# Performance work log

Measured on AMD Instinct MI355X. Metric: run time of the kernel, lower is better.

## Reference

```python
import jax, jax.numpy as jnp
import numpy as np

B = 8192   # batch
S = 115    # state dim (fixed by slice layout)
E = 3072   # retrieval embed dim
C = 128    # compressed context dim
A = 23     # action dim
NE = 4096  # number of hyperedge keys
K = 10     # top-k retrieval
TAU = 1.0  # gumbel temperature
EPS = 1e-5 # layernorm eps


def _ln(x, g, b):
    m = x.mean(-1, keepdims=True)
    v = x.var(-1, keepdims=True)
    return (x - m) * jax.lax.rsqrt(v + EPS) * g + b


def _actor(ctx, extra, w1, b1, g1, be1, w2, b2, g2, be2, w3, b3):
    x = jnp.concatenate([ctx, extra], -1)
    x = jax.nn.relu(_ln(x @ w1 + b1, g1, be1))
    x = jax.nn.relu(_ln(x @ w2 + b2, g2, be2))
    return x @ w3 + b3


def setup_inputs() -> dict:
    key = jax.random.key(0)
    ks = iter(jax.random.split(key, 80))

    def W(shape):
        return jax.random.normal(next(ks), shape, jnp.float32) * (1.0 / float(np.sqrt(shape[0])))

    inp = {}
    inp["state"] = jax.random.normal(next(ks), (B, S), jnp.float32)
    u = jax.random.uniform(next(ks), (B, 4), jnp.float32, 1e-6, 1.0 - 1e-6)
    inp["gumbel_noise"] = -jnp.log(-jnp.log(u))  # standard Gumbel samples
    inp["keys"] = jax.random.normal(next(ks), (NE, E), jnp.float32)
    # state encoder 115 -> 512 -> 512 -> 3072 + LN
    inp["se_w1"] = W((S, 512)); inp["se_b1"] = jnp.zeros(512)
    inp["se_w2"] = W((512, 512)); inp["se_b2"] = jnp.zeros(512)
    inp["se_w3"] = W((512, E)); inp["se_b3"] = jnp.zeros(E)
    inp["se_g"] = jnp.ones(E); inp["se_beta"] = jnp.zeros(E)
    # context compressor 3072 -> 512 -> 128 + LN
    inp["cc_w1"] = W((E, 512)); inp["cc_b1"] = jnp.zeros(512)
    inp["cc_w2"] = W((512, C)); inp["cc_b2"] = jnp.zeros(C)
    inp["cc_g"] = jnp.ones(C); inp["cc_beta"] = jnp.zeros(C)
    # 4 actor experts, differing only in extra-slice width
    for p, e in [("a_pre", 50), ("a_scene", 20), ("a_effect", 10), ("a_rule", 15)]:
        inp[p + "_w1"] = W((C + e, C)); inp[p + "_b1"] = jnp.zeros(C)
        inp[p + "_g1"] = jnp.ones(C); inp[p + "_be1"] = jnp.zeros(C)
        inp[p + "_w2"] = W((C, C)); inp[p + "_b2"] = jnp.zeros(C)
        inp[p + "_g2"] = jnp.ones(C); inp[p + "_be2"] = jnp.zeros(C)
        inp[p + "_w3"] = W((C, A)) * 0.01; inp[p + "_b3"] = jnp.zeros(A)  # orthogonal gain=0.01 approx
    # gumbel router 115 -> 64 -> 64 -> 4
    inp["r_w1"] = W((S, 64)); inp["r_b1"] = jnp.zeros(64)
    inp["r_w2"] = W((64, 64)); inp["r_b2"] = jnp.zeros(64)
    inp["r_w3"] = W((64, 4)); inp["r_b3"] = jnp.zeros(4)
    # critic 115 -> 256 -> 256 -> 1
    inp["c_w1"] = W((S, 256)); inp["c_b1"] = jnp.zeros(256)
    inp["c_w2"] = W((256, 256)); inp["c_b2"] = jnp.zeros(256)
    inp["c_w3"] = W((256, 1)); inp["c_b3"] = jnp.zeros(1)
    return inp


def reference(state, gumbel_noise, keys, se_w1, se_b1, se_w2, se_b2, se_w3, se_b3, se_g, se_beta, cc_w1, cc_b1, cc_w2, cc_b2, cc_g, cc_beta, a_pre_w1, a_pre_b1, a_pre_g1, a_pre_be1, a_pre_w2, a_pre_b2, a_pre_g2, a_pre_be2, a_pre_w3, a_pre_b3, a_scene_w1, a_scene_b1, a_scene_g1, a_scene_be1, a_scene_w2, a_scene_b2, a_scene_g2, a_scene_be2, a_scene_w3, a_scene_b3, a_effect_w1, a_effect_b1, a_effect_g1, a_effect_be1, a_effect_w2, a_effect_b2, a_effect_g2, a_effect_be2, a_effect_w3, a_effect_b3, a_rule_w1, a_rule_b1, a_rule_g1, a_rule_be1, a_rule_w2, a_rule_b2, a_rule_g2, a_rule_be2, a_rule_w3, a_rule_b3, r_w1, r_b1, r_w2, r_b2, r_w3, r_b3, c_w1, c_b1, c_w2, c_b2, c_w3, c_b3):
    # 1) state -> query (StateEncoder)
    q = jax.nn.relu(state @ se_w1 + se_b1)
    q = jax.nn.relu(q @ se_w2 + se_b2)
    q = _ln(q @ se_w3 + se_b3, se_g, se_beta)  # (B, E)
    # 2) top-k hard retrieval from hypergraph memory (cosine sim)
    qn = q * jax.lax.rsqrt(jnp.sum(q * q, -1, keepdims=True) + 1e-12)
    kn = keys * jax.lax.rsqrt(jnp.sum(keys * keys, -1, keepdims=True) + 1e-12)
    scores = qn @ kn.T                          # (B, NE)
    _, idx = jax.lax.top_k(scores, K)           # (B, K)
    context = jnp.take(keys, idx, axis=0).mean(1)  # (B, E) mean-pool top-k raw embeddings
    # 3) compress to shared knowledge
    h = jax.nn.relu(context @ cc_w1 + cc_b1)
    shared = _ln(h @ cc_w2 + cc_b2, cc_g, cc_beta)  # (B, C)
    # 4) state slices + 4 actor experts
    belief = state[:, :50]
    location = state[:, 20:40]
    hp = state[:, 40:50]
    inv = state[:, 45:60]
    lp = _actor(shared, belief, a_pre_w1, a_pre_b1, a_pre_g1, a_pre_be1, a_pre_w2, a_pre_b2, a_pre_g2, a_pre_be2, a_pre_w3, a_pre_b3)
    ls = _actor(shared, location, a_scene_w1, a_scene_b1, a_scene_g1, a_scene_be1, a_scene_w2, a_scene_b2, a_scene_g2, a_scene_be2, a_scene_w3, a_scene_b3)
    le = _actor(shared, hp, a_effect_w1, a_effect_b1, a_effect_g1, a_effect_be1, a_effect_w2, a_effect_b2, a_effect_g2, a_effect_be2, a_effect_w3, a_effect_b3)
    lr = _actor(shared, inv, a_rule_w1, a_rule_b1, a_rule_g1, a_rule_be1, a_rule_w2, a_rule_b2, a_rule_g2, a_rule_be2, a_rule_w3, a_rule_b3)
    # 5) gumbel-softmax hard router (straight-through)
    rh = jax.nn.relu(state @ r_w1 + r_b1)
    rh = jax.nn.relu(rh @ r_w2 + r_b2)
    rl = jnp.clip(rh @ r_w3 + r_b3, -20.0, 20.0)
    y_soft = jax.nn.softmax((rl + gumbel_noise) / TAU, -1)
    y_hard = jax.nn.one_hot(jnp.argmax(y_soft, -1), 4, dtype=y_soft.dtype)
    alpha = y_soft + jax.lax.stop_gradient(y_hard - y_soft)  # (B, 4)
    # 6) combine expert logits
    all_l = jnp.stack([lp, ls, le, lr], 1)      # (B, 4, A)
    logits = jnp.einsum('bk,bka->ba', alpha, all_l)
    # critic value
    v = jax.nn.relu(state @ c_w1 + c_b1)
    v = jax.nn.relu(v @ c_w2 + c_b2)
    value = v @ c_w3 + c_b3                      # (B, 1)
    return (logits, alpha, value)
```

## Files before the change

### kernel.cpp

```cpp
#include <hip/hip_runtime.h>

constexpr int Bz = 8192;
constexpr int Sz = 115;
constexpr int Ez = 3072;
constexpr int NEz = 4096;

typedef __attribute__((ext_vector_type(8))) short short8;
typedef __attribute__((ext_vector_type(4))) float floatx4;
typedef unsigned short ushort_t;
typedef unsigned int uint_t;

__device__ __forceinline__ ushort_t f2bf(float f) {
  uint_t u = __float_as_uint(f);
  uint_t r = (u + 0x7FFFu + ((u >> 16) & 1u)) >> 16;
  return (ushort_t)r;
}
__device__ __forceinline__ float bf2f(ushort_t b) {
  uint_t u = ((uint_t)b) << 16;
  return __uint_as_float(u);
}
__device__ __forceinline__ ushort_t f2key(float v) {
  _Float16 h = (_Float16)v;
  ushort_t b = __builtin_bit_cast(ushort_t, h);
  return b ^ ((b & 0x8000u) ? 0xFFFFu : 0x8000u);
}
__device__ __forceinline__ uint_t umax_(uint_t a, uint_t b) { return a > b ? a : b; }

__device__ __forceinline__ void gload16(const ushort_t* g, ushort_t* l) {
  __builtin_amdgcn_global_load_lds(
      (__attribute__((address_space(1))) const void*)g,
      (__attribute__((address_space(3))) void*)l, 16, 0, 0);
}

template<bool RELU, bool BIAS>
__global__ __launch_bounds__(256)
void gemm128(const float* __restrict__ A, const float* __restrict__ Bm,
             const float* __restrict__ bias, float* __restrict__ C,
             int N, int Kd)
{
  __shared__ float As[16][132];
  __shared__ float Bs[16][132];
  const int t  = threadIdx.x;
  const int tx = t & 15, ty = t >> 4;
  const int row0 = blockIdx.y * 128;
  const int col0 = blockIdx.x * 128;
  const int ar = t >> 2, ac = (t & 3) * 4;
  const int bk = t >> 5, bc = (t & 31) * 4;
  const bool a4 = (Kd & 3) == 0;

  float acc[8][8];
#pragma unroll
  for (int i = 0; i < 8; ++i)
#pragma unroll
    for (int j = 0; j < 8; ++j) acc[i][j] = 0.f;

  for (int k0 = 0; k0 < Kd; k0 += 16) {
    const bool fullA = (k0 + 16 <= Kd) && a4;
    {
      const float* ap = A + (size_t)(row0 + ar) * Kd + k0 + ac;
      if (fullA) {
        float4 v0 = *(const float4*)ap;
        float4 v1 = *(const float4*)(ap + (size_t)64 * Kd);
        As[ac + 0][ar] = v0.x; As[ac + 1][ar] = v0.y;
        As[ac + 2][ar] = v0.z; As[ac + 3][ar] = v0.w;
        As[ac + 0][ar + 64] = v1.x; As[ac + 1][ar + 64] = v1.y;
        As[ac + 2][ar + 64] = v1.z; As[ac + 3][ar + 64] = v1.w;
      } else {
#pragma unroll
        for (int e = 0; e < 4; ++e) {
          const int k = k0 + ac + e;
          float v0 = 0.f, v1 = 0.f;
          if (k < Kd) { v0 = ap[e]; v1 = ap[e + (size_t)64 * Kd]; }
          As[ac + e][ar] = v0; As[ac + e][ar + 64] = v1;
        }
      }
    }
    {
      const float* bp = Bm + (size_t)(k0 + bk) * N + col0 + bc;
      if (k0 + 16 <= Kd) {
        *(float4*)&Bs[bk][bc]     = *(const float4*)bp;
        *(float4*)&Bs[bk + 8][bc] = *(const float4*)(bp + (size_t)8 * N);
      } else {
        float4 z; z.x = z.y = z.z = z.w = 0.f;
        *(float4*)&Bs[bk][bc]     = (k0 + bk     < Kd) ? *(const float4*)bp : z;
        *(float4*)&Bs[bk + 8][bc] = (k0 + bk + 8 < Kd) ? *(const float4*)(bp + (size_t)8 * N) : z;
      }
    }
    __syncthreads();
#pragma unroll
    for (int kk = 0; kk < 16; ++kk) {
      float a[8], b[8];
      *(float4*)&a[0] = *(const float4*)&As[kk][ty * 4];
      *(float4*)&a[4] = *(const float4*)&As[kk][64 + ty * 4];
      *(float4*)&b[0] = *(const float4*)&Bs[kk][tx * 4];
      *(float4*)&b[4] = *(const float4*)&Bs[kk][64 + tx * 4];
#pragma unroll
      for (int i = 0; i < 8; ++i)
#pragma unroll
        for (int j = 0; j < 8; ++j)
          acc[i][j] = fmaf(a[i], b[j], acc[i][j]);
    }
    __syncthreads();
  }

  float bv[8];
#pragma unroll
  for (int j = 0; j < 8; ++j) bv[j] = 0.f;
  if (BIAS) {
    *(float4*)&bv[0] = *(const float4*)&bias[col0 + tx * 4];
    *(float4*)&bv[4] = *(const float4*)&bias[col0 + 64 + tx * 4];
  }
#pragma unroll
  for (int i = 0; i < 8; ++i) {
    const int r = row0 + ((i < 4) ? (ty * 4 + i) : (64 + ty * 4 + i - 4));
    float o[8];
#pragma unroll
    for (int j = 0; j < 8; ++j) {
      o[j] = acc[i][j] + bv[j];
      if (RELU) o[j] = fmaxf(o[j], 0.f);
    }
    *(float4*)&C[(size_t)r * N + col0 + tx * 4]      = *(float4*)&o[0];
    *(float4*)&C[(size_t)r * N + col0 + 64 + tx * 4] = *(float4*)&o[4];
  }
}

struct GPart {
  const float* A; const float* Bm; const float* bias;
  float* C; ushort_t* Ch; ushort_t* Cl;
  int N; int Kd; int nbx;
};

__global__ __launch_bounds__(256)
void gemm128_dual(GPart g0, GPart g1)
{
  __shared__ float As[16][132];
  __shared__ float Bs[16][132];
  const int t  = threadIdx.x;
  const int tx = t & 15, ty = t >> 4;
  const bool p0 = (int)blockIdx.x < g0.nbx;
  GPart g = p0 ? g0 : g1;
  const int bx = p0 ? blockIdx.x : (blockIdx.x - g0.nbx);
  const int row0 = blockIdx.y * 128;
  const int col0 = bx * 128;
  const int Kd = g.Kd, N = g.N;
  const int ar = t >> 2, ac = (t & 3) * 4;
  const int bk = t >> 5, bc = (t & 31) * 4;
  const bool a4 = (Kd & 3) == 0;

  float acc[8][8];
#pragma unroll
  for (int i = 0; i < 8; ++i)
#pragma unroll
    for (int j = 0; j < 8; ++j) acc[i][j] = 0.f;

  for (int k0 = 0; k0 < Kd; k0 += 16) {
    const bool fullA = (k0 + 16 <= Kd) && a4;
    {
      const float* ap = g.A + (size_t)(row0 + ar) * Kd + k0 + ac;
      if (fullA) {
        float4 v0 = *(const float4*)ap;
        float4 v1 = *(const float4*)(ap + (size_t)64 * Kd);
        As[ac + 0][ar] = v0.x; As[ac + 1][ar] = v0.y;
        As[ac + 2][ar] = v0.z; As[ac + 3][ar] = v0.w;
        As[ac + 0][ar + 64] = v1.x; As[ac + 1][ar + 64] = v1.y;
        As[ac + 2][ar + 64] = v1.z; As[ac + 3][ar + 64] = v1.w;
      } else {
#pragma unroll
        for (int e = 0; e < 4; ++e) {
          const int k = k0 + ac + e;
          float v0 = 0.f, v1 = 0.f;
          if (k < Kd) { v0 = ap[e]; v1 = ap[e + (size_t)64 * Kd]; }
          As[ac + e][ar] = v0; As[ac + e][ar + 64] = v1;
        }
      }
    }
    {
      const float* bp = g.Bm + (size_t)(k0 + bk) * N + col0 + bc;
      if (k0 + 16 <= Kd) {
        *(float4*)&Bs[bk][bc]     = *(const float4*)bp;
        *(float4*)&Bs[bk + 8][bc] = *(const float4*)(bp + (size_t)8 * N);
      } else {
        float4 z; z.x = z.y = z.z = z.w = 0.f;
        *(float4*)&Bs[bk][bc]     = (k0 + bk     < Kd) ? *(const float4*)bp : z;
        *(float4*)&Bs[bk + 8][bc] = (k0 + bk + 8 < Kd) ? *(const float4*)(bp + (size_t)8 * N) : z;
      }
    }
    __syncthreads();
#pragma unroll
    for (int kk = 0; kk < 16; ++kk) {
      float a[8], b[8];
      *(float4*)&a[0] = *(const float4*)&As[kk][ty * 4];
      *(float4*)&a[4] = *(const float4*)&As[kk][64 + ty * 4];
      *(float4*)&b[0] = *(const float4*)&Bs[kk][tx * 4];
      *(float4*)&b[4] = *(const float4*)&Bs[kk][64 + tx * 4];
#pragma unroll
      for (int i = 0; i < 8; ++i)
#pragma unroll
        for (int j = 0; j < 8; ++j)
          acc[i][j] = fmaf(a[i], b[j], acc[i][j]);
    }
    __syncthreads();
  }

  float bv[8];
  *(float4*)&bv[0] = *(const float4*)&g.bias[col0 + tx * 4];
  *(float4*)&bv[4] = *(const float4*)&g.bias[col0 + 64 + tx * 4];
#pragma unroll
  for (int i = 0; i < 8; ++i) {
    const int r = row0 + ((i < 4) ? (ty * 4 + i) : (64 + ty * 4 + i - 4));
    float o[8];
#pragma unroll
    for (int j = 0; j < 8; ++j) o[j] = fmaxf(acc[i][j] + bv[j], 0.f);
    const size_t i0 = (size_t)r * N + col0 + tx * 4;
    const size_t i1 = i0 + 64;
    if (g.C) {
      *(float4*)&g.C[i0] = *(float4*)&o[0];
      *(float4*)&g.C[i1] = *(float4*)&o[4];
    }
    if (g.Ch) {
      ushort4 h0, l0, h1, l1;
      h0.x = f2bf(o[0]); l0.x = f2bf(o[0] - bf2f(h0.x));
      h0.y = f2bf(o[1]); l0.y = f2bf(o[1] - bf2f(h0.y));
      h0.z = f2bf(o[2]); l0.z = f2bf(o[2] - bf2f(h0.z));
      h0.w = f2bf(o[3]); l0.w = f2bf(o[3] - bf2f(h0.w));
      h1.x = f2bf(o[4]); l1.x = f2bf(o[4] - bf2f(h1.x));
      h1.y = f2bf(o[5]); l1.y = f2bf(o[5] - bf2f(h1.y));
      h1.z = f2bf(o[6]); l1.z = f2bf(o[6] - bf2f(h1.z));
      h1.w = f2bf(o[7]); l1.w = f2bf(o[7] - bf2f(h1.w));
      *(ushort4*)&g.Ch[i0] = h0; *(ushort4*)&g.Cl[i0] = l0;
      *(ushort4*)&g.Ch[i1] = h1; *(ushort4*)&g.Cl[i1] = l1;
    }
  }
}

__global__ __launch_bounds__(512, 2)
void screen256(const ushort_t* __restrict__ A, const ushort_t* __restrict__ B,
               ushort_t* __restrict__ Cout, int N, int Kd)
{
  __shared__ ushort_t AL[2 * 256 * 64];
  __shared__ ushort_t BL[2 * 256 * 64];
  const int t = threadIdx.x;
  const int lane = t & 63;
  const int wid = t >> 6;
  const int wr = wid >> 2;
  const int wc = wid & 3;
  const int mr = lane & 15, qd = lane >> 4;
  const int row0 = (int)blockIdx.y << 8;
  const int col0 = (int)blockIdx.x << 8;
  const int NT = Kd >> 6;

  const int l8 = lane >> 3;
  const int c8 = (lane & 7) ^ l8;
  const ushort_t* pA = A + (size_t)(row0 + wr * 128 + wc * 16 + l8) * Kd + c8 * 8;
  const ushort_t* pB = B + (size_t)(col0 + (wid >> 1) * 64 + (wid & 1) * 16 + l8) * Kd + c8 * 8;
  ushort_t* aWp = &AL[wr * 8192 + wc * 1024];
  ushort_t* bWp = &BL[(wid >> 1) * 4096 + (wid & 1) * 1024];

  const int swz = (mr & 7) << 4;
  const int aRow = (wr * 128 + mr) * 64;
  const int bRow = (wc * 64 + mr) * 64;
  const int cu0 = ((qd * 16) ^ swz) >> 1;
  const int cu1 = ((64 + qd * 16) ^ swz) >> 1;

  floatx4 acc[8][4];
#pragma unroll
  for (int i = 0; i < 8; ++i)
#pragma unroll
    for (int j = 0; j < 4; ++j) acc[i][j] = (floatx4){0.f, 0.f, 0.f, 0.f};

  short8 A0r[4][2], A1r[4][2], B0r[2][2], B1r[2][2];

#define STA(db, h, tile) do {                                            \
    const int kt_ = ((tile) < NT ? (tile) : 0) << 6;                     \
    gload16(pA + (size_t)((h) * 64) * Kd + kt_,                          \
            aWp + (db) * 16384 + (h) * 4096);                            \
    gload16(pA + (size_t)((h) * 64 + 8) * Kd + kt_,                      \
            aWp + (db) * 16384 + (h) * 4096 + 512);                      \
  } while (0)
#define STB(db, g, tile) do {                                            \
    const int kt_ = ((tile) < NT ? (tile) : 0) << 6;                     \
    gload16(pB + (size_t)((g) * 32) * Kd + kt_,                          \
            bWp + (db) * 16384 + (g) * 2048);                            \
    gload16(pB + (size_t)((g) * 32 + 8) * Kd + kt_,                      \
            bWp + (db) * 16384 + (g) * 2048 + 512);                      \
  } while (0)
#define LDAm(dst, db, half)                                              \
  _Pragma("unroll")                                                      \
  for (int i_ = 0; i_ < 4; ++i_) {                                       \
    const int b_ = (db) * 16384 + aRow + ((half) * 4 + i_) * 1024;       \
    dst[i_][0] = *(const short8*)&AL[b_ + cu0];                          \
    dst[i_][1] = *(const short8*)&AL[b_ + cu1];                          \
  }
#define LDBm(dst, db, jh)                                                \
  _Pragma("unroll")                                                      \
  for (int j_ = 0; j_ < 2; ++j_) {                                       \
    const int b_ = (db) * 16384 + bRow + ((jh) * 2 + j_) * 1024;         \
    dst[j_][0] = *(const short8*)&BL[b_ + cu0];                          \
    dst[j_][1] = *(const short8*)&BL[b_ + cu1];                          \
  }
#define MMq(ih, jh, As_, Bs_)                                            \
  _Pragma("unroll")                                                      \
  for (int s_ = 0; s_ < 2; ++s_)                                         \
    _Pragma("unroll")                                                    \
    for (int i_ = 0; i_ < 4; ++i_)                                       \
      _Pragma("unroll")                                                  \
      for (int j_ = 0; j_ < 2; ++j_)                                     \
        acc[(ih)*4+i_][(jh)*2+j_] = __builtin_amdgcn_mfma_f32_16x16x32_bf16( \
            As_[i_][s_], Bs_[j_][s_], acc[(ih)*4+i_][(jh)*2+j_], 0, 0, 0);
#define BARM() do { __builtin_amdgcn_s_barrier();                        \
                    asm volatile("" ::: "memory"); } while (0)
#define WLG()  do { asm volatile("s_waitcnt lgkmcnt(0)" ::: "memory");   \
                    __builtin_amdgcn_sched_barrier(0); } while (0)
#define WVM(n) asm volatile("s_waitcnt vmcnt(" #n ")" ::: "memory")
#define PRIO1() __builtin_amdgcn_s_setprio(1)
#define PRIO0() __builtin_amdgcn_s_setprio(0)
#define PHASE(ih, jh, As_, Bs_, READS)                                   \
  do {                                                                   \
    __builtin_amdgcn_s_barrier(); WLG();                                 \
    PRIO1(); MMq(ih, jh, As_, Bs_); PRIO0();                             \
    READS;                                                               \
    BARM();                                                              \
  } while (0)

  STA(0, 0, 0); STB(0, 0, 0); STB(0, 1, 0); STA(0, 1, 0);
  STA(1, 0, 1); STB(1, 0, 1); STB(1, 1, 1); STA(1, 1, 1);
  WVM(8);
  BARM();
  LDAm(A0r, 0, 0); LDBm(B0r, 0, 0);

  for (int it = 0; it < NT / 2; ++it) {
    const int tp = it * 2;
    PHASE(0, 0, A0r, B0r, LDBm(B1r, 0, 1));
    STA(0, 0, tp + 2); STB(0, 0, tp + 2);
    PHASE(0, 1, A0r, B1r, LDAm(A1r, 0, 1));
    STB(0, 1, tp + 2);
    WVM(6);
    PHASE(1, 1, A1r, B1r, LDAm(A0r, 1, 0));
    STA(0, 1, tp + 2);
    PHASE(1, 0, A1r, B0r, LDBm(B1r, 1, 0));
    PHASE(0, 0, A0r, B1r, LDBm(B0r, 1, 1));
    STA(1, 0, tp + 3); STB(1, 0, tp + 3);
    PHASE(0, 1, A0r, B0r, LDAm(A1r, 1, 1));
    STB(1, 1, tp + 3);
    WVM(6);
    PHASE(1, 1, A1r, B0r, LDAm(A0r, 0, 0));
    STA(1, 1, tp + 3);
    PHASE(1, 0, A1r, B1r, LDBm(B0r, 0, 0));
  }

  asm volatile("s_waitcnt vmcnt(0) lgkmcnt(0)" ::: "memory");
  __syncthreads();

#undef STA
#undef STB
#undef LDAm
#undef LDBm
#undef MMq
#undef PHASE
#undef BARM
#undef WLG
#undef WVM
#undef PRIO1
#undef PRIO0

#pragma unroll
  for (int i = 0; i < 8; ++i) {
#pragma unroll
    for (int j = 0; j < 4; ++j) {
      const int col = col0 + wc * 64 + j * 16 + mr;
#pragma unroll
      for (int r = 0; r < 4; ++r) {
        const int row = row0 + wr * 128 + i * 16 + qd * 4 + r;
        Cout[(size_t)row * N + col] = f2key(acc[i][j][r]);
      }
    }
  }
}

template<int EPI>
__global__ __launch_bounds__(256)
void mfma3_bt(const ushort_t* __restrict__ Ah, const ushort_t* __restrict__ Alo,
              const ushort_t* __restrict__ Bh, const ushort_t* __restrict__ Blo,
              const float* __restrict__ bias, float* __restrict__ Cout,
              ushort_t* __restrict__ Ch, ushort_t* __restrict__ Cl,
              int N, int Kd)
{
  __shared__ ushort_t AhL[128 * 32];
  __shared__ ushort_t AlL[128 * 32];
  __shared__ ushort_t BhL[128 * 32];
  __shared__ ushort_t BlL[128 * 32];
  const int t = threadIdx.x;
  const int wid = t >> 6, lane = t & 63;
  const int wr = wid >> 1, wc = wid & 1;
  const int row0 = blockIdx.y * 128;
  const int col0 = blockIdx.x * 128;
  const int srow = lane >> 2;
  const int scol = (lane & 3) * 8;

  const size_t aoff0 = (size_t)(row0 + wid * 16 + srow) * Kd + scol;
  const size_t aoff1 = (size_t)(row0 + (wid + 4) * 16 + srow) * Kd + scol;
  const size_t boff0 = (size_t)(col0 + wid * 16 + srow) * Kd + scol;
  const size_t boff1 = (size_t)(col0 + (wid + 4) * 16 + srow) * Kd + scol;
  const int l0 = (wid * 16) * 32;
  const int l1 = ((wid + 4) * 16) * 32;

  const int mr = lane & 15, qd = lane >> 4;

  floatx4 acc[4][4];
#pragma unroll
  for (int i = 0; i < 4; ++i)
#pragma unroll
    for (int j = 0; j < 4; ++j) acc[i][j] = (floatx4){0.f, 0.f, 0.f, 0.f};

  for (int kb = 0; kb < Kd; kb += 32) {
    gload16(Ah + aoff0 + kb, &AhL[l0]);
    gload16(Ah + aoff1 + kb, &AhL[l1]);
    gload16(Alo + aoff0 + kb, &AlL[l0]);
    gload16(Alo + aoff1 + kb, &AlL[l1]);
    gload16(Bh + boff0 + kb, &BhL[l0]);
    gload16(Bh + boff1 + kb, &BhL[l1]);
    gload16(Blo + boff0 + kb, &BlL[l0]);
    gload16(Blo + boff1 + kb, &BlL[l1]);
    __syncthreads();
    short8 ahF[4], alF[4], bhF[4], blF[4];
#pragma unroll
    for (int i = 0; i < 4; ++i) {
      const int o = (wr * 64 + i * 16 + mr) * 32 + qd * 8;
      ahF[i] = *(const short8*)&AhL[o];
      alF[i] = *(const short8*)&AlL[o];
    }
#pragma unroll
    for (int j = 0; j < 4; ++j) {
      const int o = (wc * 64 + j * 16 + mr) * 32 + qd * 8;
      bhF[j] = *(const short8*)&BhL[o];
      blF[j] = *(const short8*)&BlL[o];
    }
#pragma unroll
    for (int i = 0; i < 4; ++i)
#pragma unroll
      for (int j = 0; j < 4; ++j) {
        acc[i][j] = __builtin_amdgcn_mfma_f32_16x16x32_bf16(alF[i], bhF[j], acc[i][j], 0, 0, 0);
        acc[i][j] = __builtin_amdgcn_mfma_f32_16x16x32_bf16(ahF[i], blF[j], acc[i][j], 0, 0, 0);
        acc[i][j] = __builtin_amdgcn_mfma_f32_16x16x32_bf16(ahF[i], bhF[j], acc[i][j], 0, 0, 0);
      }
    __syncthreads();
  }

#pragma unroll
  for (int i = 0; i < 4; ++i) {
#pragma unroll
    for (int j = 0; j < 4; ++j) {
      const int col = col0 + wc * 64 + j * 16 + mr;
#pragma unroll
      for (int r = 0; r < 4; ++r) {
        const int row = row0 + wr * 64 + i * 16 + qd * 4 + r;
        const float v = acc[i][j][r] + bias[col];
        if (EPI == 0) {
          Cout[(size_t)row * N + col] = v;
        } else {
          const float y = fmaxf(v, 0.f);
          const ushort_t h = f2bf(y);
          Ch[(size_t)row * N + col] = h;
          Cl[(size_t)row * N + col] = f2bf(y - bf2f(h));
        }
      }
    }
  }
}

__global__ __launch_bounds__(256)
void mfma_bt64(const ushort_t* __restrict__ A, const ushort_t* __restrict__ B,
               const float* __restrict__ bias, float* __restrict__ Cout,
               int N, int Kd)
{
  __shared__ ushort_t Al[2 * 64 * 32];
  __shared__ ushort_t Bl[2 * 128 * 32];
  const int t = threadIdx.x;
  const int wid = t >> 6, lane = t & 63;
  const int row0 = blockIdx.y << 6;
  const int col0 = blockIdx.x << 7;
  const int srow = lane >> 2;
  const int scol = (lane & 3) * 8;
  const int mr = lane & 15, qd = lane >> 4;

  const ushort_t* gsrc[6];
  ushort_t* ldst[6];
#pragma unroll
  for (int m = 0; m < 6; ++m) {
    const int c = wid * 6 + m;
    if (c < 8) {
      const int sub = c >> 2, grp = c & 3;
      gsrc[m] = A + (size_t)(row0 + grp * 16 + srow) * Kd + sub * 32 + scol;
      ldst[m] = &Al[sub * 2048 + (grp * 16 + srow) * 32];
    } else {
      const int b = c - 8, sub = b >> 3, grp = b & 7;
      gsrc[m] = B + (size_t)(col0 + grp * 16 + srow) * Kd + sub * 32 + scol;
      ldst[m] = &Bl[sub * 4096 + (grp * 16 + srow) * 32];
    }
  }

  floatx4 acc[4][2];
#pragma unroll
  for (int i = 0; i < 4; ++i)
#pragma unroll
    for (int j = 0; j < 2; ++j) acc[i][j] = (floatx4){0.f, 0.f, 0.f, 0.f};

  for (int kb = 0; kb < Kd; kb += 64) {
#pragma unroll
    for (int m = 0; m < 6; ++m) gload16(gsrc[m] + kb, ldst[m]);
    __syncthreads();
#pragma unroll
    for (int sub = 0; sub < 2; ++sub) {
      short8 aF[4], bF[2];
#pragma unroll
      for (int i = 0; i < 4; ++i)
        aF[i] = *(const short8*)&Al[sub * 2048 + (i * 16 + mr) * 32 + qd * 8];
#pragma unroll
      for (int j = 0; j < 2; ++j)
        bF[j] = *(const short8*)&Bl[sub * 4096 + (wid * 32 + j * 16 + mr) * 32 + qd * 8];
#pragma unroll
      for (int i = 0; i < 4; ++i)
#pragma unroll
        for (int j = 0; j < 2; ++j)
          acc[i][j] = __builtin_amdgcn_mfma_f32_16x16x32_bf16(aF[i], bF[j], acc[i][j], 0, 0, 0);
    }
    __syncthreads();
  }

#pragma unroll
  for (int i = 0; i < 4; ++i) {
#pragma unroll
    for (int j = 0; j < 2; ++j) {
      const int col = col0 + wid * 32 + j * 16 + mr;
#pragma unroll
      for (int r = 0; r < 4; ++r) {
        const int row = row0 + i * 16 + qd * 4 + r;
        Cout[(size_t)row * N + col] = fmaxf(acc[i][j][r] + bias[col], 0.f);
      }
    }
  }
}

__global__ __launch_bounds__(256)
void gemm_scores(const float* __restrict__ A, const float* __restrict__ Bm,
                 const float* __restrict__ rk, ushort_t* __restrict__ S)
{
  __shared__ float As[16][132];
  __shared__ float Bs[16][132];
  const int t  = threadIdx.x;
  const int tx = t & 15, ty = t >> 4;
  const int row0 = blockIdx.y * 128;
  const int col0 = blockIdx.x * 128;
  const int ar = t >> 2, ac = (t & 3) * 4;
  const int Kd = Ez;

  float acc[8][8];
#pragma unroll
  for (int i = 0; i < 8; ++i)
#pragma unroll
    for (int j = 0; j < 8; ++j) acc[i][j] = 0.f;

  for (int k0 = 0; k0 < Kd; k0 += 16) {
    {
      const float* ap = A + (size_t)(row0 + ar) * Kd + k0 + ac;
      float4 v0 = *(const float4*)ap;
      float4 v1 = *(const float4*)(ap + (size_t)64 * Kd);
      As[ac + 0][ar] = v0.x; As[ac + 1][ar] = v0.y;
      As[ac + 2][ar] = v0.z; As[ac + 3][ar] = v0.w;
      As[ac + 0][ar + 64] = v1.x; As[ac + 1][ar + 64] = v1.y;
      As[ac + 2][ar + 64] = v1.z; As[ac + 3][ar + 64] = v1.w;
    }
    {
      const float* bp = Bm + (size_t)(col0 + ar) * Kd + k0 + ac;
      float4 v0 = *(const float4*)bp;
      float4 v1 = *(const float4*)(bp + (size_t)64 * Kd);
      Bs[ac + 0][ar] = v0.x; Bs[ac + 1][ar] = v0.y;
      Bs[ac + 2][ar] = v0.z; Bs[ac + 3][ar] = v0.w;
      Bs[ac + 0][ar + 64] = v1.x; Bs[ac + 1][ar + 64] = v1.y;
      Bs[ac + 2][ar + 64] = v1.z; Bs[ac + 3][ar + 64] = v1.w;
    }
    __syncthreads();
#pragma unroll
    for (int kk = 0; kk < 16; ++kk) {
      float a[8], b[8];
      *(float4*)&a[0] = *(const float4*)&As[kk][ty * 4];
      *(float4*)&a[4] = *(const float4*)&As[kk][64 + ty * 4];
      *(float4*)&b[0] = *(const float4*)&Bs[kk][tx * 4];
      *(float4*)&b[4] = *(const float4*)&Bs[kk][64 + tx * 4];
#pragma unroll
      for (int i = 0; i < 8; ++i)
#pragma unroll
        for (int j = 0; j < 8; ++j)
          acc[i][j] = fmaf(a[i], b[j], acc[i][j]);
    }
    __syncthreads();
  }

  float rk0[8];
  *(float4*)&rk0[0] = *(const float4*)&rk[col0 + tx * 4];
  *(float4*)&rk0[4] = *(const float4*)&rk[col0 + 64 + tx * 4];
#pragma unroll
  for (int i = 0; i < 8; ++i) {
    const int r = row0 + ((i < 4) ? (ty * 4 + i) : (64 + ty * 4 + i - 4));
    ushort4 h0, h1;
    h0.x = f2key(acc[i][0] * rk0[0]); h0.y = f2key(acc[i][1] * rk0[1]);
    h0.z = f2key(acc[i][2] * rk0[2]); h0.w = f2key(acc[i][3] * rk0[3]);
    h1.x = f2key(acc[i][4] * rk0[4]); h1.y = f2key(acc[i][5] * rk0[5]);
    h1.z = f2key(acc[i][6] * rk0[6]); h1.w = f2key(acc[i][7] * rk0[7]);
    *(ushort4*)&S[(size_t)r * NEz + col0 + tx * 4]      = h0;
    *(ushort4*)&S[(size_t)r * NEz + col0 + 64 + tx * 4] = h1;
  }
}

struct LN4 {
  const float* W[4]; const float* b[4]; const float* g[4]; const float* be[4];
  int eoff[4]; int elen[4];
};

template<bool RELU, bool HASEXT>
__global__ __launch_bounds__(256)
void gemm_ln4(const float* __restrict__ A1base, size_t a1stride, int K1,
              const float* __restrict__ A2, LN4 p,
              float* __restrict__ outbase, size_t ostride)
{
  __shared__ float As[32][68];
  __shared__ float Bs[32][132];
  __shared__ float rsum[64][17];
  __shared__ float rsq[64][17];
  __shared__ float stm[64], str[64];
  const int a = blockIdx.y;
  const float* A1 = A1base + (size_t)a * a1stride;
  float* out = outbase + (size_t)a * ostride;
  const float* W = p.W[a];
  const float* bias = p.b[a];
  const float* g = p.g[a];
  const float* be = p.be[a];
  const int eoff = HASEXT ? p.eoff[a] : 0;
  const int K2 = HASEXT ? p.elen[a] : 0;

  const int t = threadIdx.x;
  const int tx = t & 15, ty = t >> 4;
  const int row0 = blockIdx.x * 64;
  const int Kt = K1 + K2;
  const int ar = t >> 2, ac = (t & 3) * 8;
  const int bk = t >> 3, bc = (t & 7) * 16;

  float acc[4][8];
#pragma unroll
  for (int i = 0; i < 4; ++i)
#pragma unroll
    for (int j = 0; j < 8; ++j) acc[i][j] = 0.f;

  for (int k0 = 0; k0 < Kt; k0 += 32) {
    const int grow = row0 + ar;
#pragma unroll
    for (int e = 0; e < 8; ++e) {
      const int k = k0 + ac + e;
      float v = 0.f;
      if (k < K1)      v = A1[(size_t)grow * K1 + k];
      else if (k < Kt) v = A2[(size_t)grow * 115 + eoff + (k - K1)];
      As[ac + e][ar] = v;
    }
    {
      const int k = k0 + bk;
#pragma unroll
      for (int qd = 0; qd < 4; ++qd) {
        float4 z; z.x = z.y = z.z = z.w = 0.f;
        *(float4*)&Bs[bk][bc + 4 * qd] =
            (k < Kt) ? *(const float4*)&W[(size_t)k * 128 + bc + 4 * qd] : z;
      }
    }
    __syncthreads();
#pragma unroll
    for (int kk = 0; kk < 32; ++kk) {
      float av[4], bv2[8];
      *(float4*)&av[0]  = *(const float4*)&As[kk][ty * 4];
      *(float4*)&bv2[0] = *(const float4*)&Bs[kk][tx * 4];
      *(float4*)&bv2[4] = *(const float4*)&Bs[kk][64 + tx * 4];
#pragma unroll
      for (int i = 0; i < 4; ++i)
#pragma unroll
        for (int j = 0; j < 8; ++j)
          acc[i][j] = fmaf(av[i], bv2[j], acc[i][j]);
    }
    __syncthreads();
  }

  float bv[8];
  *(float4*)&bv[0] = *(const float4*)&bias[tx * 4];
  *(float4*)&bv[4] = *(const float4*)&bias[64 + tx * 4];
#pragma unroll
  for (int i = 0; i < 4; ++i) {
    float s = 0.f, q = 0.f;
#pragma unroll
    for (int j = 0; j < 8; ++j) {
      acc[i][j] += bv[j];
      s += acc[i][j];
      q += acc[i][j] * acc[i][j];
    }
    rsum[ty * 4 + i][tx] = s;
    rsq[ty * 4 + i][tx]  = q;
  }
  __syncthreads();
  if (t < 64) {
    float s = 0.f, q = 0.f;
#pragma unroll
    for (int x = 0; x < 16; ++x) { s += rsum[t][x]; q += rsq[t][x]; }
    const float m = s * (1.f / 128.f);
    const float v = q * (1.f / 128.f) - m * m;
    stm[t] = m;
    str[t] = rsqrtf(v + 1e-5f);
  }
  __syncthreads();
#pragma unroll
  for (int i = 0; i < 4; ++i) {
    const int r = ty * 4 + i;
    const float m = stm[r], rs = str[r];
    float o[8];
#pragma unroll
    for (int j = 0; j < 8; ++j) {
      const int col = (j < 4) ? (tx * 4 + j) : (64 + tx * 4 + (j - 4));
      float y = (acc[i][j] - m) * rs * g[col] + be[col];
      if (RELU) y = fmaxf(y, 0.f);
      o[j] = y;
    }
    *(float4*)&out[(size_t)(row0 + r) * 128 + tx * 4]      = *(float4*)&o[0];
    *(float4*)&out[(size_t)(row0 + r) * 128 + 64 + tx * 4] = *(float4*)&o[4];
  }
}

__device__ __forceinline__ float blockSum256(float v, float* sh)
{
#pragma unroll
  for (int d = 32; d; d >>= 1) v += __shfl_down(v, d, 64);
  __syncthreads();
  if ((threadIdx.x & 63) == 0) sh[threadIdx.x >> 6] = v;
  __syncthreads();
  return sh[0] + sh[1] + sh[2] + sh[3];
}

__global__ __launch_bounds__(256)
void norm_cvt_fused(float* __restrict__ q, const float* __restrict__ g,
                    const float* __restrict__ be, ushort_t* __restrict__ qb,
                    const float* __restrict__ keys, float* __restrict__ rk,
                    ushort_t* __restrict__ knb)
{
  __shared__ float sh[4];
  const int b = blockIdx.x, t = threadIdx.x;
  if (b < Bz) {
    const int row = b;
    float* qr = q + (size_t)row * Ez;
    float x[12];
#pragma unroll
    for (int i = 0; i < 12; ++i) x[i] = qr[t + (i << 8)];
    float s = 0.f;
#pragma unroll
    for (int i = 0; i < 12; ++i) s += x[i];
    const float m = blockSum256(s, sh) * (1.f / (float)Ez);
    float vs = 0.f;
#pragma unroll
    for (int i = 0; i < 12; ++i) { const float d = x[i] - m; vs += d * d; }
    const float v = blockSum256(vs, sh) * (1.f / (float)Ez);
    const float rs = rsqrtf(v + 1e-5f);
    float y[12]; float qs = 0.f;
#pragma unroll
    for (int i = 0; i < 12; ++i) {
      const int c = t + (i << 8);
      const float yy = (x[i] - m) * rs * g[c] + be[c];
      y[i] = yy; qs += yy * yy;
    }
    const float tot = blockSum256(qs, sh);
    const float s2 = rsqrtf(tot + 1e-12f);
#pragma unroll
    for (int i = 0; i < 12; ++i) {
      const int c = t + (i << 8);
      const float yn = y[i] * s2;
      qr[c] = yn;
      qb[(size_t)row * Ez + c] = f2bf(yn);
    }
  } else {
    const int row = b - Bz;
    const float* xr = keys + (size_t)row * Ez;
    float x[12]; float qs = 0.f;
#pragma unroll
    for (int i = 0; i < 12; ++i) { x[i] = xr[t + (i << 8)]; qs += x[i] * x[i]; }
    const float tot = blockSum256(qs, sh);
    const float s = rsqrtf(tot + 1e-12f);
    if (t == 0) rk[row] = s;
#pragma unroll
    for (int i = 0; i < 12; ++i)
      knb[(size_t)row * Ez + t + (i << 8)] = f2bf(x[i] * s);
  }
}

__global__ __launch_bounds__(256)
void ln_l2_q(float* __restrict__ q, const float* __restrict__ g,
             const float* __restrict__ be)
{
  __shared__ float sh[4];
  const int row = blockIdx.x, t = threadIdx.x;
  float* qr = q + (size_t)row * Ez;
  float x[12];
#pragma unroll
  for (int i = 0; i < 12; ++i) x[i] = qr[t + (i << 8)];
  float s = 0.f;
#pragma unroll
  for (int i = 0; i < 12; ++i) s += x[i];
  const float m = blockSum256(s, sh) * (1.f / (float)Ez);
  float vs = 0.f;
#pragma unroll
  for (int i = 0; i < 12; ++i) { const float d = x[i] - m; vs += d * d; }
  const float v = blockSum256(vs, sh) * (1.f / (float)Ez);
  const float rs = rsqrtf(v + 1e-5f);
  float y[12]; float qs = 0.f;
#pragma unroll
  for (int i = 0; i < 12; ++i) {
    const int c = t + (i << 8);
    const float yy = (x[i] - m) * rs * g[c] + be[c];
    y[i] = yy; qs += yy * yy;
  }
  const float tot = blockSum256(qs, sh);
  const float s2 = rsqrtf(tot + 1e-12f);
#pragma unroll
  for (int i = 0; i < 12; ++i) qr[t + (i << 8)] = y[i] * s2;
}

__global__ __launch_bounds__(256)
void keynorm(const float* __restrict__ keys, float* __restrict__ rk)
{
  __shared__ float sh[4];
  const int row = blockIdx.x, t = threadIdx.x;
  const float* xr = keys + (size_t)row * Ez;
  float qs = 0.f;
#pragma unroll
  for (int i = 0; i < 12; ++i) { const float x = xr[t + (i << 8)]; qs += x * x; }
  const float tot = blockSum256(qs, sh);
  if (t == 0) rk[row] = rsqrtf(tot + 1e-12f);
}

__global__ __launch_bounds__(256)
void wt_split2(const float* __restrict__ w2, ushort_t* __restrict__ h2,
               ushort_t* __restrict__ l2v,
               const float* __restrict__ w3, ushort_t* __restrict__ h3,
               ushort_t* __restrict__ l3v)
{
  __shared__ float tile[64][65];
  const float* w; ushort_t* hT; ushort_t* lT; int C; int n0;
  if ((int)blockIdx.y < 8) { w = w2; hT = h2; lT = l2v; C = 512;  n0 = blockIdx.y * 64; }
  else                     { w = w3; hT = h3; lT = l3v; C = 3072; n0 = (blockIdx.y - 8) * 64; }
  const int k0 = blockIdx.x * 64;
  const int t = threadIdx.x;
  const int c = t & 63, r4 = t >> 6;
#pragma unroll
  for (int rr = 0; rr < 16; ++rr) {
    const int r = rr * 4 + r4;
    tile[r][c] = w[(size_t)(k0 + r) * C + n0 + c];
  }
  __syncthreads();
#pragma unroll
  for (int rr = 0; rr < 16; ++rr) {
    const int n = rr * 4 + r4;
    const float a = tile[c][n];
    const ushort_t h = f2bf(a);
    hT[(size_t)(n0 + n) * 512 + k0 + c] = h;
    lT[(size_t)(n0 + n) * 512 + k0 + c] = f2bf(a - bf2f(h));
  }
}

__global__ __launch_bounds__(256)
void cvt_w1t_t(const float* __restrict__ w, ushort_t* __restrict__ out)
{
  __shared__ float tile[64][65];
  const int k0 = blockIdx.x * 64;
  const int n0 = blockIdx.y * 64;
  const int t = threadIdx.x;
  const int c = t & 63, r4 = t >> 6;
#pragma unroll
  for (int rr = 0; rr < 16; ++rr) {
    const int r = rr * 4 + r4;
    tile[r][c] = w[(size_t)(k0 + r) * 512 + n0 + c];
  }
  __syncthreads();
#pragma unroll
  for (int rr = 0; rr < 16; ++rr) {
    const int n = rr * 4 + r4;
    out[(size_t)(n0 + n) * Ez + k0 + c] = f2bf(tile[c][n]);
  }
}

__global__ __launch_bounds__(256)
void topk16(const ushort_t* __restrict__ S, int* __restrict__ outIdx)
{
  __shared__ uint_t cand[64];
  const int row = blockIdx.x, t = threadIdx.x;
  const int w = t >> 6, lane = t & 63;
  const int base = (w << 10) + (lane << 4);
  const ushort_t* sr = S + (size_t)row * NEz + base;
  uint4 v0 = *(const uint4*)sr;
  uint4 v1 = *(const uint4*)(sr + 8);
  const uint_t cb = (uint_t)(4095 - base);
  uint_t p[16];
  p[0]  = ((v0.x & 0xFFFFu) << 12) | (cb - 0);
  p[1]  = ((v0.x >> 16)     << 12) | (cb - 1);
  p[2]  = ((v0.y & 0xFFFFu) << 12) | (cb - 2);
  p[3]  = ((v0.y >> 16)     << 12) | (cb - 3);
  p[4]  = ((v0.z & 0xFFFFu) << 12) | (cb - 4);
  p[5]  = ((v0.z >> 16)     << 12) | (cb - 5);
  p[6]  = ((v0.w & 0xFFFFu) << 12) | (cb - 6);
  p[7]  = ((v0.w >> 16)     << 12) | (cb - 7);
  p[8]  = ((v1.x & 0xFFFFu) << 12) | (cb - 8);
  p[9]  = ((v1.x >> 16)     << 12) | (cb - 9);
  p[10] = ((v1.y & 0xFFFFu) << 12) | (cb - 10);
  p[11] = ((v1.y >> 16)     << 12) | (cb - 11);
  p[12] = ((v1.z & 0xFFFFu) << 12) | (cb - 12);
  p[13] = ((v1.z >> 16)     << 12) | (cb - 13);
  p[14] = ((v1.w & 0xFFFFu) << 12) | (cb - 14);
  p[15] = ((v1.w >> 16)     << 12) | (cb - 15);

  for (int it = 0; it < 16; ++it) {
    uint_t m = p[0];
#pragma unroll
    for (int j = 1; j < 16; ++j) m = umax_(m, p[j]);
#pragma unroll
    for (int d = 1; d < 64; d <<= 1)
      m = umax_(m, (uint_t)__shfl_xor((int)m, d, 64));
    if (lane == it) cand[(w << 4) + it] = m;
#pragma unroll
    for (int j = 0; j < 16; ++j) p[j] = (p[j] == m) ? 0u : p[j];
  }
  __syncthreads();
  if (t < 64) {
    uint_t mine = cand[t];
    for (int it = 0; it < 16; ++it) {
      uint_t m = mine;
#pragma unroll
      for (int d = 1; d < 64; d <<= 1)
        m = umax_(m, (uint_t)__shfl_xor((int)m, d, 64));
      if (t == it) outIdx[(size_t)row * 16 + it] = 4095 - (int)(m & 0xFFFu);
      mine = (mine == m) ? 0u : mine;
    }
  }
}

template<bool BFOUT>
__global__ __launch_bounds__(256)
void rescore_gather(const float* __restrict__ qn, const float* __restrict__ keys,
                    const float* __restrict__ rk, const int* __restrict__ cand,
                    void* __restrict__ ctxOut)
{
  __shared__ float qs[Ez];
  __shared__ double sv[16];
  __shared__ int si[16];
  __shared__ int sel10[10];
  const int row = blockIdx.x, t = threadIdx.x;
  const int w = t >> 6, lane = t & 63;

  {
    const float* qr = qn + (size_t)row * Ez;
#pragma unroll
    for (int i = 0; i < 3; ++i) {
      const int c = (t << 2) + (i << 10);
      *(float4*)&qs[c] = *(const float4*)&qr[c];
    }
  }
  __syncthreads();

#pragma unroll
  for (int cc = 0; cc < 4; ++cc) {
    const int slot = w * 4 + cc;
    const int id = cand[(size_t)row * 16 + slot];
    const float* kr = keys + (size_t)id * Ez;
    double s = 0.0;
#pragma unroll
    for (int it = 0; it < 12; ++it) {
      const int c = (lane << 2) + (it << 8);
      float4 k4 = *(const float4*)&kr[c];
      float4 q4 = *(const float4*)&qs[c];
      s += (double)q4.x * (double)k4.x;
      s += (double)q4.y * (double)k4.y;
      s += (double)q4.z * (double)k4.z;
      s += (double)q4.w * (double)k4.w;
    }
#pragma unroll
    for (int d = 32; d; d >>= 1) s += __shfl_down(s, d, 64);
    if (lane == 0) { sv[slot] = s * (double)rk[id]; si[slot] = id; }
  }
  __syncthreads();

  if (t == 0) {
    for (int it = 0; it < 10; ++it) {
      int bj = 0; double bvv = sv[0]; int bi = si[0];
      for (int j = 1; j < 16; ++j) {
        const double v = sv[j]; const int i2 = si[j];
        if (v > bvv || (v == bvv && i2 < bi)) { bj = j; bvv = v; bi = i2; }
      }
      sel10[it] = bi;
      sv[bj] = -1e300;
    }
  }
  __syncthreads();

  int id[10];
#pragma unroll
  for (int j = 0; j < 10; ++j) id[j] = sel10[j];

#pragma unroll
  for (int i = 0; i < 3; ++i) {
    const int c = (t << 2) + (i << 10);
    float4 a = {0.f, 0.f, 0.f, 0.f};
#pragma unroll
    for (int j = 0; j < 10; ++j) {
      float4 v = *(const float4*)&keys[(size_t)id[j] * Ez + c];
      a.x += v.x; a.y += v.y; a.z += v.z; a.w += v.w;
    }
    if (BFOUT) {
      ushort4 o;
      o.x = f2bf(a.x * 0.1f); o.y = f2bf(a.y * 0.1f);
      o.z = f2bf(a.z * 0.1f); o.w = f2bf(a.w * 0.1f);
      *(ushort4*)&((ushort_t*)ctxOut)[(size_t)row * Ez + c] = o;
    } else {
      float4 o;
      o.x = a.x * 0.1f; o.y = a.y * 0.1f; o.z = a.z * 0.1f; o.w = a.w * 0.1f;
      *(float4*)&((float*)ctxOut)[(size_t)row * Ez + c] = o;
    }
  }
}

__global__ __launch_bounds__(256)
void router_kernel(const float* __restrict__ state, const float* __restrict__ gn,
                   const float* __restrict__ w1, const float* __restrict__ b1,
                   const float* __restrict__ w2, const float* __restrict__ b2,
                   const float* __restrict__ w3, const float* __restrict__ b3,
                   float* __restrict__ outAlpha)
{
  const int row = blockIdx.x * 256 + threadIdx.x;
  const float* sr = state + (size_t)row * Sz;
  float h1[64];
#pragma unroll
  for (int j = 0; j < 64; ++j) h1[j] = b1[j];
  for (int k = 0; k < Sz; ++k) {
    const float a = sr[k];
    const float* wr = w1 + (size_t)k * 64;
#pragma unroll
    for (int j = 0; j < 64; ++j) h1[j] = fmaf(a, wr[j], h1[j]);
  }
#pragma unroll
  for (int j = 0; j < 64; ++j) h1[j] = fmaxf(h1[j], 0.f);
  float h2[64];
#pragma unroll
  for (int j = 0; j < 64; ++j) h2[j] = b2[j];
#pragma unroll
  for (int k = 0; k < 64; ++k) {
    const float a = h1[k];
    const float* wr = w2 + (size_t)k * 64;
#pragma unroll
    for (int j = 0; j < 64; ++j) h2[j] = fmaf(a, wr[j], h2[j]);
  }
#pragma unroll
  for (int j = 0; j < 64; ++j) h2[j] = fmaxf(h2[j], 0.f);
  float z[4];
#pragma unroll
  for (int a = 0; a < 4; ++a) {
    float s = b3[a];
#pragma unroll
    for (int k = 0; k < 64; ++k) s = fmaf(h2[k], w3[k * 4 + a], s);
    s = fminf(fmaxf(s, -20.f), 20.f);
    z[a] = s + gn[(size_t)row * 4 + a];
  }
  float mz = z[0];
#pragma unroll
  for (int a = 1; a < 4; ++a) mz = fmaxf(mz, z[a]);
  float e[4]; float se = 0.f;
#pragma unroll
  for (int a = 0; a < 4; ++a) { e[a] = expf(z[a] - mz); se += e[a]; }
  const float inv = 1.f / se;
  float y[4];
#pragma unroll
  for (int a = 0; a < 4; ++a) y[a] = e[a] * inv;
  int am = 0;
#pragma unroll
  for (int a = 1; a < 4; ++a) if (y[a] > y[am]) am = a;
#pragma unroll
  for (int a = 0; a < 4; ++a) {
    const float hard = (a == am) ? 1.f : 0.f;
    outAlpha[(size_t)row * 4 + a] = y[a] + (hard - y[a]);
  }
}

__global__ __launch_bounds__(256)
void critic_head(const float* __restrict__ c2, const float* __restrict__ w3,
                 const float* __restrict__ b3, float* __restrict__ outv)
{
  const int t = threadIdx.x;
  const int w = t >> 6, lane = t & 63;
  const int row0 = blockIdx.x * 64 + w * 16;
  float wv[4];
  *(float4*)&wv[0] = *(const float4*)&w3[lane * 4];
  const float b0 = b3[0];
#pragma unroll
  for (int rr = 0; rr < 16; ++rr) {
    const int row = row0 + rr;
    float4 x = *(const float4*)&c2[(size_t)row * 256 + lane * 4];
    float s = x.x * wv[0] + x.y * wv[1] + x.z * wv[2] + x.w * wv[3];
#pragma unroll
    for (int d = 32; d; d >>= 1) s += __shfl_down(s, d, 64);
    if (lane == 0) outv[row] = s + b0;
  }
}

struct HeadP { const float* w3[4]; const float* b3[4]; };

__global__ __launch_bounds__(256)
void actor_head4(const float* __restrict__ x2g, HeadP p,
                 const float* __restrict__ alpha, float* __restrict__ outL)
{
  __shared__ float wsm[4][128 * 23];
  __shared__ float bs[4][23];
  const int t = threadIdx.x;
#pragma unroll
  for (int a = 0; a < 4; ++a) {
    for (int i = t; i < 128 * 23; i += 256) wsm[a][i] = p.w3[a][i];
    if (t < 23) bs[a][t] = p.b3[a][t];
  }
  __syncthreads();
  const int row = blockIdx.x * 32 + (t >> 3);
  const int cg = t & 7;
  float sum[3] = {0.f, 0.f, 0.f};
#pragma unroll
  for (int a = 0; a < 4; ++a) {
    const float al = alpha[(size_t)row * 4 + a];
    const float* xr = x2g + (size_t)a * Bz * 128 + (size_t)row * 128;
    float acc[3] = {0.f, 0.f, 0.f};
    for (int kk = 0; kk < 128; ++kk) {
      const float xa = xr[kk];
#pragma unroll
      for (int j = 0; j < 3; ++j) {
        const int col = cg + 8 * j;
        if (col < 23) acc[j] = fmaf(xa, wsm[a][kk * 23 + col], acc[j]);
      }
    }
#pragma unroll
    for (int j = 0; j < 3; ++j) {
      const int col = cg + 8 * j;
      if (col < 23) sum[j] += al * (acc[j] + bs[a][col]);
    }
  }
#pragma unroll
  for (int j = 0; j < 3; ++j) {
    const int col = cg + 8 * j;
    if (col < 23) outL[(size_t)row * 23 + col] = sum[j];
  }
}

extern "C" void kernel_launch(void* const* d_in, const int* in_sizes, int n_in,
                              void* d_out, int out_size, void* d_ws, size_t ws_size,
                              hipStream_t stream)
{
  const float* state  = (const float*)d_in[0];
  const float* gumbel = (const float*)d_in[1];
  const float* keys   = (const float*)d_in[2];
  const float* se_w1 = (const float*)d_in[3];
  const float* se_b1 = (const float*)d_in[4];
  const float* se_w2 = (const float*)d_in[5];
  const float* se_b2 = (const float*)d_in[6];
  const float* se_w3 = (const float*)d_in[7];
  const float* se_b3 = (const float*)d_in[8];
  const float* se_g  = (const float*)d_in[9];
  const float* se_be = (const float*)d_in[10];
  const float* cc_w1 = (const float*)d_in[11];
  const float* cc_b1 = (const float*)d_in[12];
  const float* cc_w2 = (const float*)d_in[13];
  const float* cc_b2 = (const float*)d_in[14];
  const float* cc_g  = (const float*)d_in[15];
  const float* cc_be = (const float*)d_in[16];
  const float* r_w1 = (const float*)d_in[57];
  const float* r_b1 = (const float*)d_in[58];
  const float* r_w2 = (const float*)d_in[59];
  const float* r_b2 = (const float*)d_in[60];
  const float* r_w3 = (const float*)d_in[61];
  const float* r_b3 = (const float*)d_in[62];
  const float* c_w1 = (const float*)d_in[63];
  const float* c_b1 = (const float*)d_in[64];
  const float* c_w2 = (const float*)d_in[65];
  const float* c_b2 = (const float*)d_in[66];
  const float* c_w3 = (const float*)d_in[67];
  const float* c_b3 = (const float*)d_in[68];

  float* wsf = (float*)d_ws;
  const size_t qF = (size_t)Bz * Ez;
  const size_t uF = (size_t)16777216;
  float* q = wsf;
  float* U = wsf + qF;
  ushort_t* sAh  = (ushort_t*)(U + 0);
  ushort_t* sAl  = (ushort_t*)(U + 2097152);
  ushort_t* sBh  = (ushort_t*)(U + 4194304);
  ushort_t* sBl  = (ushort_t*)(U + 6291456);
  ushort_t* w3hT = (ushort_t*)(U + 8388608);
  ushort_t* w3lT = (ushort_t*)(U + 9175040);
  ushort_t* w2hT = (ushort_t*)(U + 9961472);
  ushort_t* w2lT = (ushort_t*)(U + 10092544);
  float* sA = U;
  float* sB = U + 4194304;
  ushort_t* scoresU = (ushort_t*)U;
  ushort_t* ctxb = (ushort_t*)U;
  float* cch = U + 12582912;
  float* shr = U;
  float* x1g = U + 1 * 1048576;
  float* x2g = U + 5 * 1048576;
  float* cr1 = q;
  float* cr2 = q + 2097152;
  ushort_t* qbf  = (ushort_t*)(wsf + qF + uF);
  ushort_t* knbf = qbf + qF;
  ushort_t* w1T  = knbf + (size_t)NEz * Ez;
  const size_t bfHalves = qF + (size_t)NEz * Ez + (size_t)512 * Ez;
  const size_t baseBytes = (qF + uF) * sizeof(float);
  const size_t tailBytes = 4096 * 4 + (size_t)Bz * 16 * 4;
  const bool fast = ws_size >= baseBytes + bfHalves * 2 + tailBytes;
  float* tailF = (float*)((char*)d_ws + (fast ? baseBytes + bfHalves * 2 : baseBytes));
  float* rk  = tailF;
  int* cand  = (int*)(tailF + 4096);

  float* outL = (float*)d_out;
  float* outA = outL + (size_t)Bz * 23;
  float* outV = outA + (size_t)Bz * 4;

  const dim3 blk(256);

  {
    GPart e0 = {state, se_w1, se_b1, fast ? nullptr : sA,
                fast ? sAh : nullptr, fast ? sAl : nullptr, 512, 115, 4};
    GPart e1 = {state, c_w1, c_b1, cr1, nullptr, nullptr, 256, 115, 2};
    gemm128_dual<<<dim3(6, 64), blk, 0, stream>>>(e0, e1);
  }
  gemm128<true, true><<<dim3(2, 64), blk, 0, stream>>>(cr1, c_w2, c_b2, cr2, 256, 256);

  if (fast) {
    wt_split2<<<dim3(8, 56), blk, 0, stream>>>(se_w2, w2hT, w2lT, se_w3, w3hT, w3lT);
    mfma3_bt<1><<<dim3(4, 64), blk, 0, stream>>>(sAh, sAl, w2hT, w2lT, se_b2,
                                                 nullptr, sBh, sBl, 512, 512);
  } else {
    gemm128<true, true><<<dim3(4, 64), blk, 0, stream>>>(sA, se_w2, se_b2, sB, 512, 512);
  }

  critic_head<<<dim3(128), blk, 0, stream>>>(cr2, c_w3, c_b3, outV);
  router_kernel<<<dim3(32), blk, 0, stream>>>(state, gumbel, r_w1, r_b1, r_w2, r_b2,
                                              r_w3, r_b3, outA);

  if (fast) {
    mfma3_bt<0><<<dim3(24, 64), blk, 0, stream>>>(sBh, sBl, w3hT, w3lT, se_b3,
                                                  q, nullptr, nullptr, 3072, 512);
    norm_cvt_fused<<<dim3(Bz + NEz), blk, 0, stream>>>(q, se_g, se_be, qbf,
                                                       keys, rk, knbf);
    cvt_w1t_t<<<dim3(48, 8), blk, 0, stream>>>(cc_w1, w1T);
    screen256<<<dim3(16, 32), dim3(512), 0, stream>>>(qbf, knbf, scoresU, NEz, Ez);
  } else {
    gemm128<false, true><<<dim3(24, 64), blk, 0, stream>>>(sB, se_w3, se_b3, q, 3072, 512);
    ln_l2_q<<<dim3(Bz), blk, 0, stream>>>(q, se_g, se_be);
    keynorm<<<dim3(NEz), blk, 0, stream>>>(keys, rk);
    gemm_scores<<<dim3(32, 64), blk, 0, stream>>>(q, keys, rk, scoresU);
  }

  topk16<<<dim3(Bz), blk, 0, stream>>>(scoresU, cand);

  if (fast) {
    rescore_gather<true><<<dim3(Bz), blk, 0, stream>>>(q, keys, rk, cand, ctxb);
    mfma_bt64<<<dim3(4, 128), blk, 0, stream>>>(ctxb, w1T, cc_b1, cch, 512, Ez);
  } else {
    rescore_gather<false><<<dim3(Bz), blk, 0, stream>>>(q, keys, rk, cand, q);
    gemm128<true, true><<<dim3(4, 64), blk, 0, stream>>>(q, cc_w1, cc_b1, cch, 512, Ez);
  }
  {
    LN4 pcc = {};
    pcc.W[0] = cc_w2; pcc.b[0] = cc_b2; pcc.g[0] = cc_g; pcc.be[0] = cc_be;
    gemm_ln4<false, false><<<dim3(128, 1), blk, 0, stream>>>(cch, 0, 512, nullptr, pcc,
                                                             shr, 0);
  }

  {
    LN4 p1 = {}, p2 = {};
    HeadP ph = {};
    const int eoffs[4] = {0, 20, 40, 45};
    const int elens[4] = {50, 20, 10, 15};
    for (int a = 0; a < 4; ++a) {
      const int base = 17 + 10 * a;
      p1.W[a]  = (const float*)d_in[base + 0];
      p1.b[a]  = (const float*)d_in[base + 1];
      p1.g[a]  = (const float*)d_in[base + 2];
      p1.be[a] = (const float*)d_in[base + 3];
      p1.eoff[a] = eoffs[a]; p1.elen[a] = elens[a];
      p2.W[a]  = (const float*)d_in[base + 4];
      p2.b[a]  = (const float*)d_in[base + 5];
      p2.g[a]  = (const float*)d_in[base + 6];
      p2.be[a] = (const float*)d_in[base + 7];
      ph.w3[a] = (const float*)d_in[base + 8];
      ph.b3[a] = (const float*)d_in[base + 9];
    }
    gemm_ln4<true, true ><<<dim3(128, 4), blk, 0, stream>>>(shr, 0, 128, state, p1,
                                                            x1g, (size_t)Bz * 128);
    gemm_ln4<true, false><<<dim3(128, 4), blk, 0, stream>>>(x1g, (size_t)Bz * 128, 128,
                                                            nullptr, p2,
                                                            x2g, (size_t)Bz * 128);
    actor_head4<<<dim3(256), blk, 0, stream>>>(x2g, ph, outA, outL);
  }
}
```

Measured before the change: 1.264 ms.

## Merge GEMM pipeline phases into two half-tile phases per k-step

Restructures the software-pipelined bf16 MFMA main loop of the similarity GEMM. Each k-step now runs two phases instead of four, each issuing MFMAs for a full half of the A rows against both B halves. The global-to-LDS stores and the LDS fragment reads are rescheduled to match. This halves the barriers per k-step and gives longer MFMA bursts. In exchange it loads more register fragments per phase, which raises register pressure, and moves the vmcnt waits into each phase, which may expose load latency.

```diff
diff --git a/kernel.cpp b/kernel.cpp
--- a/kernel.cpp
+++ b/kernel.cpp
@@ -314,38 +314,32 @@
 #define WVM(n) asm volatile("s_waitcnt vmcnt(" #n ")" ::: "memory")
 #define PRIO1() __builtin_amdgcn_s_setprio(1)
 #define PRIO0() __builtin_amdgcn_s_setprio(0)
-#define PHASE(ih, jh, As_, Bs_, READS)                                   \
+#define PHASE2(ih, READS)                                                \
   do {                                                                   \
+    WVM(8);                                                              \
     __builtin_amdgcn_s_barrier(); WLG();                                 \
-    PRIO1(); MMq(ih, jh, As_, Bs_); PRIO0();                             \
+    PRIO1(); MMq(ih, 0, (ih ? A1r : A0r), B0r);                          \
+             MMq(ih, 1, (ih ? A1r : A0r), B1r); PRIO0();                 \
     READS;                                                               \
     BARM();                                                              \
   } while (0)
 
   STA(0, 0, 0); STB(0, 0, 0); STB(0, 1, 0); STA(0, 1, 0);
-  STA(1, 0, 1); STB(1, 0, 1); STB(1, 1, 1); STA(1, 1, 1);
-  WVM(8);
+  STA(1, 0, 1); STB(1, 0, 1); STB(1, 1, 1);
+  WVM(6);
   BARM();
-  LDAm(A0r, 0, 0); LDBm(B0r, 0, 0);
+  LDAm(A0r, 0, 0); LDBm(B0r, 0, 0); LDBm(B1r, 0, 1);
 
   for (int it = 0; it < NT / 2; ++it) {
     const int tp = it * 2;
-    PHASE(0, 0, A0r, B0r, LDBm(B1r, 0, 1));
-    STA(0, 0, tp + 2); STB(0, 0, tp + 2);
-    PHASE(0, 1, A0r, B1r, LDAm(A1r, 0, 1));
-    STB(0, 1, tp + 2);
-    WVM(6);
-    PHASE(1, 1, A1r, B1r, LDAm(A0r, 1, 0));
+    STA(1, 1, tp + 1);
+    PHASE2(0, LDAm(A1r, 0, 1));
+    STA(0, 0, tp + 2); STB(0, 0, tp + 2); STB(0, 1, tp + 2);
+    PHASE2(1, LDAm(A0r, 1, 0); LDBm(B0r, 1, 0); LDBm(B1r, 1, 1));
     STA(0, 1, tp + 2);
-    PHASE(1, 0, A1r, B0r, LDBm(B1r, 1, 0));
-    PHASE(0, 0, A0r, B1r, LDBm(B0r, 1, 1));
-    STA(1, 0, tp + 3); STB(1, 0, tp + 3);
-    PHASE(0, 1, A0r, B0r, LDAm(A1r, 1, 1));
-    STB(1, 1, tp + 3);
-    WVM(6);
-    PHASE(1, 1, A1r, B0r, LDAm(A0r, 0, 0));
-    STA(1, 1, tp + 3);
-    PHASE(1, 0, A1r, B1r, LDBm(B0r, 0, 0));
+    PHASE2(0, LDAm(A1r, 1, 1));
+    STA(1, 0, tp + 3); STB(1, 0, tp + 3); STB(1, 1, tp + 3);
+    PHASE2(1, LDAm(A0r, 0, 0); LDBm(B0r, 0, 0); LDBm(B1r, 0, 1));
   }
 
   asm volatile("s_waitcnt vmcnt(0) lgkmcnt(0)" ::: "memory");
@@ -356,7 +350,7 @@
 #undef LDAm
 #undef LDBm
 #undef MMq
-#undef PHASE
+#undef PHASE2
 #undef BARM
 #undef WLG
 #undef WVM
```

New measurement: 1.227 ms. -2.9%, faster.
